# Kernel tuning notes

Measured on AMD Instinct MI355X. Metric: run time of the kernel, lower is better.

The kernel has to match this reference:

```python
import jax, jax.numpy as jnp
import numpy as np

N_NODES = 100000
N_EDGES = 3200000
IN_CH = 32
HID = 16


def setup_inputs() -> dict:
    key = jax.random.key(0)
    ks = jax.random.split(key, 8)
    x = jax.random.normal(ks[0], (N_NODES, IN_CH), dtype=jnp.float32)
    edge_index = jax.random.randint(ks[1], (2, N_EDGES), 0, N_NODES, dtype=jnp.int64)
    s1 = 1.0 / np.sqrt(IN_CH)
    s2 = 1.0 / np.sqrt(HID)
    Wl1 = jax.random.normal(ks[2], (HID, IN_CH), dtype=jnp.float32) * s1
    Wr1 = jax.random.normal(ks[3], (HID, IN_CH), dtype=jnp.float32) * s1
    b1 = jnp.zeros((HID,), dtype=jnp.float32)
    Wl2 = jax.random.normal(ks[4], (1, HID), dtype=jnp.float32) * s2
    Wr2 = jax.random.normal(ks[5], (1, HID), dtype=jnp.float32) * s2
    b2 = jnp.zeros((1,), dtype=jnp.float32)
    return {"x": x, "edge_index": edge_index, "Wl1": Wl1, "Wr1": Wr1,
            "b1": b1, "Wl2": Wl2, "Wr2": Wr2, "b2": b2}


def _sage_conv(h, src, dst, deg_inv, Wl, Wr, b):
    # mean aggregation of source features at destination nodes
    msg_sum = jax.ops.segment_sum(h[src], dst, num_segments=N_NODES)  # [N, F]
    agg = msg_sum * deg_inv[:, None]
    # lin_l(agg) + lin_r(h): lin_l carries the bias (PyG SAGEConv convention)
    return agg @ Wl.T + b + h @ Wr.T


def reference(x, edge_index, Wl1, Wr1, b1, Wl2, Wr2, b2):
    src = edge_index[0]
    dst = edge_index[1]
    deg = jax.ops.segment_sum(jnp.ones((N_EDGES,), dtype=x.dtype), dst,
                              num_segments=N_NODES)
    deg_inv = 1.0 / jnp.maximum(deg, 1.0)  # mean; nodes w/o in-edges get 0 agg

    h = _sage_conv(x, src, dst, deg_inv, Wl1, Wr1, b1)
    h = jax.nn.relu(h)
    # F.dropout in eval mode -> identity
    out = _sage_conv(h, src, dst, deg_inv, Wl2, Wr2, b2)
    return out.squeeze(-1)  # [N]
```

## Files before the change

### kernel.cpp

```cpp
#include <hip/hip_runtime.h>

#define N_NODES 100000
#define N_EDGES 3200000
#define NB 1024
#define BKN 98
#define RSZ 3968
#define TILE 6250
#define NTILES 512
#define MAXIT 13
#define MAXB 8
#define PROJ_BLOCKS 196

typedef float f32x4 __attribute__((ext_vector_type(4)));


__device__ __forceinline__ float bf2f_lo(unsigned int w) {
  return __uint_as_float(w << 16);
}
__device__ __forceinline__ float bf2f_hi(unsigned int w) {
  return __uint_as_float(w & 0xFFFF0000u);
}
__device__ __forceinline__ unsigned short f2bf(float f) {
  unsigned int b = __float_as_uint(f);
  return (unsigned short)((b + 0x7FFFu + ((b >> 16) & 1u)) >> 16);
}

__global__ __launch_bounds__(512, 4) void k_countproj(
    const float* __restrict__ x, const int* __restrict__ ei,
    const float* __restrict__ Wl1, const float* __restrict__ Wr1,
    const float* __restrict__ b1, unsigned short* __restrict__ p1h,
    float* __restrict__ q1b, int* __restrict__ cnt) {
  __shared__ union {
    int hist[1024];
    struct { float Wl[512], Wr[512], b[16]; } w;
  } u;
  const int t = threadIdx.x;
  const int kb = blockIdx.x;

  if (kb < NTILES) {
    for (int i = t; i < 1024; i += 512) u.hist[i] = 0;
    __syncthreads();
    const int tb = kb * TILE;
#pragma unroll
    for (int i = 0; i < MAXIT; ++i) {
      const int pos = t + i * 512;
      if (pos < TILE) {
        const int d = ei[N_EDGES + tb + pos];
        atomicAdd(&u.hist[(int)((unsigned)d / (unsigned)BKN)], 1);
      }
    }
    __syncthreads();
    ((int2*)(cnt + kb * NB))[t] = make_int2(u.hist[2 * t], u.hist[2 * t + 1]);
    return;
  }

  u.w.Wl[t] = Wl1[t];
  u.w.Wr[t] = Wr1[t];
  if (t < 16) u.w.b[t] = b1[t];
  __syncthreads();

  const int n = (kb - NTILES) * 512 + t;
  if (n >= N_NODES) return;

  float xr[32];
  const float4* xp = (const float4*)(x + (size_t)n * 32);
#pragma unroll
  for (int j = 0; j < 8; ++j) {
    float4 v = xp[j];
    xr[4 * j + 0] = v.x;
    xr[4 * j + 1] = v.y;
    xr[4 * j + 2] = v.z;
    xr[4 * j + 3] = v.w;
  }
  float pv[16], qv[16];
#pragma unroll
  for (int hh = 0; hh < 16; ++hh) {
    float a = 0.f, b = 0.f;
#pragma unroll
    for (int i = 0; i < 32; ++i) {
      a = fmaf(xr[i], u.w.Wl[hh * 32 + i], a);
      b = fmaf(xr[i], u.w.Wr[hh * 32 + i], b);
    }
    pv[hh] = a;
    qv[hh] = b + u.w.b[hh];
  }
  unsigned int w[8];
#pragma unroll
  for (int j = 0; j < 8; ++j)
    w[j] = (unsigned int)f2bf(pv[2 * j]) |
           ((unsigned int)f2bf(pv[2 * j + 1]) << 16);
  uint4* pp = (uint4*)(p1h + (size_t)n * 16);
  pp[0] = make_uint4(w[0], w[1], w[2], w[3]);
  pp[1] = make_uint4(w[4], w[5], w[6], w[7]);
  float4* qp = (float4*)(q1b + (size_t)n * 16);
#pragma unroll
  for (int j = 0; j < 4; ++j)
    qp[j] = make_float4(qv[4 * j], qv[4 * j + 1], qv[4 * j + 2], qv[4 * j + 3]);
}

__global__ __launch_bounds__(512) void k_scan(const int* __restrict__ cnt,
                                              int* __restrict__ offs,
                                              int* __restrict__ tot) {
  const int t = threadIdx.x;
  const int lane = t & 63;
  const int b = blockIdx.x * 8 + (t >> 6);
  int carry = 0;
#pragma unroll
  for (int c = 0; c < 8; ++c) {
    const int tile = c * 64 + lane;
    const int v = cnt[tile * NB + b];
    int incl = v;
#pragma unroll
    for (int o = 1; o < 64; o <<= 1) {
      const int uu = __shfl_up(incl, o);
      if (lane >= o) incl += uu;
    }
    offs[b * NTILES + tile] = carry + incl - v;
    carry += __shfl(incl, 63);
  }
  if (lane == 0) tot[b] = carry;
}

__global__ __launch_bounds__(512, 4) void k_scatter(const int* __restrict__ ei,
                                                    const int* __restrict__ offs,
                                                    int* __restrict__ recs) {
  __shared__ int hist[1024];
  __shared__ int delta[NB];
  __shared__ int wsum[8];
  __shared__ int stage[TILE];
  __shared__ unsigned short bid[TILE + 6];
  const int t = threadIdx.x;
  const int kb = blockIdx.x;
  for (int i = t; i < 1024; i += 512) hist[i] = 0;
  __syncthreads();

  const int tb = kb * TILE;
  int rec[MAXIT], aux[MAXIT];
#pragma unroll
  for (int i = 0; i < MAXIT; ++i) {
    const int pos = t + i * 512;
    if (pos < TILE) {
      const int e = tb + pos;
      const int s = ei[e];
      const int d = ei[N_EDGES + e];
      const int k = (int)((unsigned)d / (unsigned)BKN);
      const int rank = atomicAdd(&hist[k], 1);
      rec[i] = ((d - k * BKN) << 17) | s;
      aux[i] = (k << 16) | rank;
    } else {
      aux[i] = -1;
    }
  }
  __syncthreads();

  const int s0 = hist[2 * t], s1 = hist[2 * t + 1];
  const int sp = s0 + s1;
  int incl = sp;
#pragma unroll
  for (int o = 1; o < 64; o <<= 1) {
    const int uu = __shfl_up(incl, o);
    if ((t & 63) >= o) incl += uu;
  }
  if ((t & 63) == 63) wsum[t >> 6] = incl;
  __syncthreads();
  if (t == 0) {
    int run = 0;
#pragma unroll
    for (int i = 0; i < 8; ++i) {
      const int v = wsum[i];
      wsum[i] = run;
      run += v;
    }
  }
  __syncthreads();
  const int ex = wsum[t >> 6] + incl - sp;
  hist[2 * t] = ex;
  hist[2 * t + 1] = ex + s0;
  {
    const int b = 2 * t;
    delta[b] = b * RSZ + offs[b * NTILES + kb] - ex;
    delta[b + 1] = (b + 1) * RSZ + offs[(b + 1) * NTILES + kb] - (ex + s0);
  }
  __syncthreads();

#pragma unroll
  for (int i = 0; i < MAXIT; ++i) {
    if (aux[i] >= 0) stage[hist[aux[i] >> 16] + (aux[i] & 0xFFFF)] = rec[i];
  }
  for (int k2 = t; k2 < NB; k2 += 512) {
    const int st = hist[k2];
    const int en = (k2 == NB - 1) ? TILE : hist[k2 + 1];
    for (int p = st; p < en; ++p) bid[p] = (unsigned short)k2;
  }
  __syncthreads();

  for (int pos = t; pos < TILE; pos += 512) {
    const int bb = bid[pos];
    const int idx = delta[bb] + pos;
    if (idx < (bb + 1) * RSZ) recs[idx] = stage[pos];
  }
}

__global__ __launch_bounds__(512, 8) void k_sortagg1(
    const int* __restrict__ tot, const int* __restrict__ recs,
    const unsigned short* __restrict__ p1h, const float* __restrict__ q1b,
    const float* __restrict__ Wl2, const float* __restrict__ Wr2,
    float* __restrict__ p2, float* __restrict__ r2,
    float* __restrict__ deg_inv) {
  __shared__ int hist[128];
  __shared__ int nstart[128];
  __shared__ int ssort[RSZ];
  __shared__ float sWl[16], sWr[16];
  const int t = threadIdx.x;
  const int kb = blockIdx.x;
  const int b0 = kb * RSZ;
  const int cend = min(tot[kb], RSZ);
  if (t < 128) hist[t] = 0;
  if (t < 16) {
    sWl[t] = Wl2[t];
    sWr[t] = Wr2[t];
  }
  __syncthreads();

  int rc[MAXB], ax[MAXB];
#pragma unroll
  for (int i = 0; i < MAXB; ++i) {
    const int r = t + i * 512;
    if (r < cend) {
      const int rv = recs[b0 + r];
      const int local = rv >> 17;
      const int rank = atomicAdd(&hist[local], 1);
      rc[i] = rv & 0x1FFFF;
      ax[i] = (local << 13) | rank;
    } else {
      ax[i] = -1;
    }
  }
  __syncthreads();

  if (t < 64) {
    const int a = hist[t], b = hist[t + 64];
    int ia = a, ib = b;
#pragma unroll
    for (int o = 1; o < 64; o <<= 1) {
      const int ua = __shfl_up(ia, o);
      const int ub = __shfl_up(ib, o);
      if (t >= o) {
        ia += ua;
        ib += ub;
      }
    }
    const int tt = __shfl(ia, 63);
    nstart[t] = ia - a;
    nstart[t + 64] = tt + ib - b;
  }
  __syncthreads();

#pragma unroll
  for (int i = 0; i < MAXB; ++i) {
    if (ax[i] >= 0) ssort[nstart[ax[i] >> 13] + (ax[i] & 0x1FFF)] = rc[i];
  }
  __syncthreads();

  const int quad = t & 3;
  const int half = quad & 1;
  const int epar = quad >> 1;
  const unsigned short* pb = p1h + half * 8;
  const int local = t >> 2;
  if (local < BKN) {
    const int n = kb * BKN + local;
    if (n < N_NODES) {
      const int st = nstart[local];
      const int k = hist[local];

      float acc[8];
#pragma unroll
      for (int i = 0; i < 8; ++i) acc[i] = 0.f;
      int j = epar;
      for (; j + 6 < k; j += 8) {
        const int s0 = ssort[st + j], s1 = ssort[st + j + 2],
                  s2 = ssort[st + j + 4], s3 = ssort[st + j + 6];
        const uint4 w0 = *(const uint4*)(pb + (size_t)s0 * 16);
        const uint4 w1 = *(const uint4*)(pb + (size_t)s1 * 16);
        const uint4 w2 = *(const uint4*)(pb + (size_t)s2 * 16);
        const uint4 w3 = *(const uint4*)(pb + (size_t)s3 * 16);
        acc[0] +=
            (bf2f_lo(w0.x) + bf2f_lo(w1.x)) + (bf2f_lo(w2.x) + bf2f_lo(w3.x));
        acc[1] +=
            (bf2f_hi(w0.x) + bf2f_hi(w1.x)) + (bf2f_hi(w2.x) + bf2f_hi(w3.x));
        acc[2] +=
            (bf2f_lo(w0.y) + bf2f_lo(w1.y)) + (bf2f_lo(w2.y) + bf2f_lo(w3.y));
        acc[3] +=
            (bf2f_hi(w0.y) + bf2f_hi(w1.y)) + (bf2f_hi(w2.y) + bf2f_hi(w3.y));
        acc[4] +=
            (bf2f_lo(w0.z) + bf2f_lo(w1.z)) + (bf2f_lo(w2.z) + bf2f_lo(w3.z));
        acc[5] +=
            (bf2f_hi(w0.z) + bf2f_hi(w1.z)) + (bf2f_hi(w2.z) + bf2f_hi(w3.z));
        acc[6] +=
            (bf2f_lo(w0.w) + bf2f_lo(w1.w)) + (bf2f_lo(w2.w) + bf2f_lo(w3.w));
        acc[7] +=
            (bf2f_hi(w0.w) + bf2f_hi(w1.w)) + (bf2f_hi(w2.w) + bf2f_hi(w3.w));
      }
      for (; j < k; j += 2) {
        const uint4 w = *(const uint4*)(pb + (size_t)ssort[st + j] * 16);
        acc[0] += bf2f_lo(w.x);
        acc[1] += bf2f_hi(w.x);
        acc[2] += bf2f_lo(w.y);
        acc[3] += bf2f_hi(w.y);
        acc[4] += bf2f_lo(w.z);
        acc[5] += bf2f_hi(w.z);
        acc[6] += bf2f_lo(w.w);
        acc[7] += bf2f_hi(w.w);
      }
#pragma unroll
      for (int i = 0; i < 8; ++i) acc[i] += __shfl_xor(acc[i], 2);

      const float di = 1.f / fmaxf((float)k, 1.f);
      const float4* qp = (const float4*)(q1b + (size_t)n * 16 + half * 8);
      const float4 qa = qp[0], qb = qp[1];
      float h[8];
      h[0] = fmaxf(fmaf(acc[0], di, qa.x), 0.f);
      h[1] = fmaxf(fmaf(acc[1], di, qa.y), 0.f);
      h[2] = fmaxf(fmaf(acc[2], di, qa.z), 0.f);
      h[3] = fmaxf(fmaf(acc[3], di, qa.w), 0.f);
      h[4] = fmaxf(fmaf(acc[4], di, qb.x), 0.f);
      h[5] = fmaxf(fmaf(acc[5], di, qb.y), 0.f);
      h[6] = fmaxf(fmaf(acc[6], di, qb.z), 0.f);
      h[7] = fmaxf(fmaf(acc[7], di, qb.w), 0.f);
      float pa = 0.f, pbv = 0.f;
#pragma unroll
      for (int i = 0; i < 8; ++i) {
        pa = fmaf(h[i], sWl[half * 8 + i], pa);
        pbv = fmaf(h[i], sWr[half * 8 + i], pbv);
      }
      pa += __shfl_xor(pa, 1);
      pbv += __shfl_xor(pbv, 1);
      if (quad == 0) {
        p2[n] = pa;
        r2[n] = pbv;
        deg_inv[n] = di;
      }
    }
  }
}

__global__ __launch_bounds__(512, 8) void k_agg2out(
    const int* __restrict__ tot, const int* __restrict__ recs,
    const float* __restrict__ p2, const float* __restrict__ r2,
    const float* __restrict__ deg_inv, const float* __restrict__ b2,
    float* __restrict__ out) {
  __shared__ float acc[BKN];
  const int t = threadIdx.x;
  const int kb = blockIdx.x;
  if (t < BKN) acc[t] = 0.f;
  __syncthreads();

  const int b0 = kb * RSZ;
  const int cnt = min(tot[kb], RSZ);
  int r = t;
  for (; r + 1536 < cnt; r += 2048) {
    const int rv0 = recs[b0 + r];
    const int rv1 = recs[b0 + r + 512];
    const int rv2 = recs[b0 + r + 1024];
    const int rv3 = recs[b0 + r + 1536];
    const float v0 = p2[rv0 & 0x1FFFF];
    const float v1 = p2[rv1 & 0x1FFFF];
    const float v2 = p2[rv2 & 0x1FFFF];
    const float v3 = p2[rv3 & 0x1FFFF];
    atomicAdd(&acc[rv0 >> 17], v0);
    atomicAdd(&acc[rv1 >> 17], v1);
    atomicAdd(&acc[rv2 >> 17], v2);
    atomicAdd(&acc[rv3 >> 17], v3);
  }
  for (; r < cnt; r += 512) {
    const int rv = recs[b0 + r];
    atomicAdd(&acc[rv >> 17], p2[rv & 0x1FFFF]);
  }
  __syncthreads();

  if (t < BKN) {
    const int n = kb * BKN + t;
    if (n < N_NODES) out[n] = fmaf(acc[t], deg_inv[n], r2[n] + b2[0]);
  }
}

extern "C" void kernel_launch(void* const* d_in, const int* in_sizes, int n_in,
                              void* d_out, int out_size, void* d_ws,
                              size_t ws_size, hipStream_t stream) {
  const float* x   = (const float*)d_in[0];
  const int*   ei  = (const int*)d_in[1];
  const float* Wl1 = (const float*)d_in[2];
  const float* Wr1 = (const float*)d_in[3];
  const float* b1  = (const float*)d_in[4];
  const float* Wl2 = (const float*)d_in[5];
  const float* Wr2 = (const float*)d_in[6];
  const float* b2  = (const float*)d_in[7];
  float* out = (float*)d_out;

  const size_t N = N_NODES;
  int* wi = (int*)d_ws;
  int* cnt  = wi;
  int* offs = cnt + NTILES * NB;
  int* tot  = offs + NB * NTILES;
  int* recs = tot + NB;
  unsigned short* p1h = (unsigned short*)(recs + (size_t)NB * RSZ);
  float* q1b     = (float*)(p1h + 16 * N);
  float* p2      = q1b + 16 * N;
  float* r2      = p2 + N;
  float* deg_inv = r2 + N;

  k_countproj<<<NTILES + PROJ_BLOCKS, 512, 0, stream>>>(x, ei, Wl1, Wr1, b1,
                                                        p1h, q1b, cnt);
  k_scan<<<NB / 8, 512, 0, stream>>>(cnt, offs, tot);
  k_scatter<<<NTILES, 512, 0, stream>>>(ei, offs, recs);
  k_sortagg1<<<NB, 512, 0, stream>>>(tot, recs, p1h, q1b, Wl2, Wr2, p2, r2,
                                     deg_inv);
  k_agg2out<<<NB, 512, 0, stream>>>(tot, recs, p2, r2, deg_inv, b2, out);
}
```

Measured before the change: 176.4 us.

## Fuse both aggregation stages into a cooperative kernel and restructure scatter tiles

Merges the layer-1 sort/aggregate and layer-2 aggregate/output kernels into one cooperative kernel with a grid-wide sync. The second stage reuses the per-bucket sorted edge lists, degree and root term already in LDS instead of re-reading records and global arrays. The scatter kernel now uses larger 1024-thread tiles with a two-pass count-then-place sort, and writes 16-aligned padded runs with hole records as int4 stores. The cost is extra padding slots, a larger RSZ, and a reliance on cooperative launch residency, with the old two-kernel path kept as a fallback.

```diff
diff --git a/kernel.cpp b/kernel.cpp
--- a/kernel.cpp
+++ b/kernel.cpp
@@ -1,17 +1,19 @@
 #include <hip/hip_runtime.h>
+#include <hip/hip_cooperative_groups.h>
+
+namespace cg = cooperative_groups;
 
 #define N_NODES 100000
 #define N_EDGES 3200000
 #define NB 1024
 #define BKN 98
-#define RSZ 3968
-#define TILE 6250
-#define NTILES 512
-#define MAXIT 13
-#define MAXB 8
+#define RSZ 5120
+#define TILE 12500
+#define NTILES 256
+#define MAXITC 25
+#define MAXB 10
 #define PROJ_BLOCKS 196
-
-typedef float f32x4 __attribute__((ext_vector_type(4)));
+#define HOLE_REC (127 << 17)
 
 
 __device__ __forceinline__ float bf2f_lo(unsigned int w) {
@@ -42,7 +44,7 @@
     __syncthreads();
     const int tb = kb * TILE;
 #pragma unroll
-    for (int i = 0; i < MAXIT; ++i) {
+    for (int i = 0; i < MAXITC; ++i) {
       const int pos = t + i * 512;
       if (pos < TILE) {
         const int d = ei[N_EDGES + tb + pos];
@@ -106,113 +108,109 @@
   const int b = blockIdx.x * 8 + (t >> 6);
   int carry = 0;
 #pragma unroll
-  for (int c = 0; c < 8; ++c) {
+  for (int c = 0; c < 4; ++c) {
     const int tile = c * 64 + lane;
-    const int v = cnt[tile * NB + b];
-    int incl = v;
+    const int pv = (cnt[tile * NB + b] + 15) & ~15;
+    int incl = pv;
 #pragma unroll
     for (int o = 1; o < 64; o <<= 1) {
       const int uu = __shfl_up(incl, o);
       if (lane >= o) incl += uu;
     }
-    offs[b * NTILES + tile] = carry + incl - v;
+    offs[b * NTILES + tile] = carry + incl - pv;
     carry += __shfl(incl, 63);
   }
   if (lane == 0) tot[b] = carry;
 }
 
-__global__ __launch_bounds__(512, 4) void k_scatter(const int* __restrict__ ei,
-                                                    const int* __restrict__ offs,
-                                                    int* __restrict__ recs) {
+__global__ __launch_bounds__(1024, 1) void k_scatter(
+    const int* __restrict__ ei, const int* __restrict__ offs,
+    int* __restrict__ recs) {
   __shared__ int hist[1024];
-  __shared__ int delta[NB];
-  __shared__ int wsum[8];
+  __shared__ int bstart[1024];
+  __shared__ int wsum[16];
   __shared__ int stage[TILE];
-  __shared__ unsigned short bid[TILE + 6];
   const int t = threadIdx.x;
   const int kb = blockIdx.x;
-  for (int i = t; i < 1024; i += 512) hist[i] = 0;
+  hist[t] = 0;
   __syncthreads();
 
   const int tb = kb * TILE;
-  int rec[MAXIT], aux[MAXIT];
-#pragma unroll
-  for (int i = 0; i < MAXIT; ++i) {
-    const int pos = t + i * 512;
+#pragma unroll
+  for (int i = 0; i < 13; ++i) {
+    const int pos = t + i * 1024;
+    if (pos < TILE) {
+      const int d = ei[N_EDGES + tb + pos];
+      atomicAdd(&hist[(int)((unsigned)d / (unsigned)BKN)], 1);
+    }
+  }
+  __syncthreads();
+
+  const int sv = hist[t];
+  int incl = sv;
+#pragma unroll
+  for (int o = 1; o < 64; o <<= 1) {
+    const int uu = __shfl_up(incl, o);
+    if ((t & 63) >= o) incl += uu;
+  }
+  if ((t & 63) == 63) wsum[t >> 6] = incl;
+  __syncthreads();
+  if (t == 0) {
+    int run = 0;
+#pragma unroll
+    for (int i = 0; i < 16; ++i) {
+      const int v = wsum[i];
+      wsum[i] = run;
+      run += v;
+    }
+  }
+  __syncthreads();
+  bstart[t] = wsum[t >> 6] + incl - sv;
+  hist[t] = 0;
+  __syncthreads();
+
+#pragma unroll
+  for (int i = 0; i < 13; ++i) {
+    const int pos = t + i * 1024;
     if (pos < TILE) {
       const int e = tb + pos;
       const int s = ei[e];
       const int d = ei[N_EDGES + e];
       const int k = (int)((unsigned)d / (unsigned)BKN);
-      const int rank = atomicAdd(&hist[k], 1);
-      rec[i] = ((d - k * BKN) << 17) | s;
-      aux[i] = (k << 16) | rank;
-    } else {
-      aux[i] = -1;
-    }
-  }
-  __syncthreads();
-
-  const int s0 = hist[2 * t], s1 = hist[2 * t + 1];
-  const int sp = s0 + s1;
-  int incl = sp;
-#pragma unroll
-  for (int o = 1; o < 64; o <<= 1) {
-    const int uu = __shfl_up(incl, o);
-    if ((t & 63) >= o) incl += uu;
-  }
-  if ((t & 63) == 63) wsum[t >> 6] = incl;
-  __syncthreads();
-  if (t == 0) {
-    int run = 0;
-#pragma unroll
-    for (int i = 0; i < 8; ++i) {
-      const int v = wsum[i];
-      wsum[i] = run;
-      run += v;
-    }
-  }
-  __syncthreads();
-  const int ex = wsum[t >> 6] + incl - sp;
-  hist[2 * t] = ex;
-  hist[2 * t + 1] = ex + s0;
+      const int r = atomicAdd(&hist[k], 1);
+      stage[bstart[k] + r] = ((d - k * BKN) << 17) | s;
+    }
+  }
+  __syncthreads();
+
   {
-    const int b = 2 * t;
-    delta[b] = b * RSZ + offs[b * NTILES + kb] - ex;
-    delta[b + 1] = (b + 1) * RSZ + offs[(b + 1) * NTILES + kb] - (ex + s0);
-  }
-  __syncthreads();
-
-#pragma unroll
-  for (int i = 0; i < MAXIT; ++i) {
-    if (aux[i] >= 0) stage[hist[aux[i] >> 16] + (aux[i] & 0xFFFF)] = rec[i];
-  }
-  for (int k2 = t; k2 < NB; k2 += 512) {
-    const int st = hist[k2];
-    const int en = (k2 == NB - 1) ? TILE : hist[k2 + 1];
-    for (int p = st; p < en; ++p) bid[p] = (unsigned short)k2;
-  }
-  __syncthreads();
-
-  for (int pos = t; pos < TILE; pos += 512) {
-    const int bb = bid[pos];
-    const int idx = delta[bb] + pos;
-    if (idx < (bb + 1) * RSZ) recs[idx] = stage[pos];
-  }
-}
-
-__global__ __launch_bounds__(512, 8) void k_sortagg1(
-    const int* __restrict__ tot, const int* __restrict__ recs,
-    const unsigned short* __restrict__ p1h, const float* __restrict__ q1b,
-    const float* __restrict__ Wl2, const float* __restrict__ Wr2,
-    float* __restrict__ p2, float* __restrict__ r2,
-    float* __restrict__ deg_inv) {
-  __shared__ int hist[128];
-  __shared__ int nstart[128];
-  __shared__ int ssort[RSZ];
-  __shared__ float sWl[16], sWr[16];
-  const int t = threadIdx.x;
-  const int kb = blockIdx.x;
+    const int b = t;
+    const int c = hist[b];
+    const int st = bstart[b];
+    const int off = offs[b * NTILES + kb];
+    const int pc = (c + 15) & ~15;
+    int* gb = recs + (size_t)b * RSZ + off;
+    for (int i = 0; i < pc; i += 4) {
+      if (off + i + 4 <= RSZ) {
+        int4 v;
+        v.x = (i < c) ? stage[st + i] : HOLE_REC;
+        v.y = (i + 1 < c) ? stage[st + i + 1] : HOLE_REC;
+        v.z = (i + 2 < c) ? stage[st + i + 2] : HOLE_REC;
+        v.w = (i + 3 < c) ? stage[st + i + 3] : HOLE_REC;
+        *(int4*)(gb + i) = v;
+      }
+    }
+  }
+}
+
+template <bool FUSED>
+__device__ __forceinline__ void sortagg_body(
+    const int t, const int kb, const int* __restrict__ tot,
+    const int* __restrict__ recs, const unsigned short* __restrict__ p1h,
+    const float* __restrict__ q1b, const float* __restrict__ Wl2,
+    const float* __restrict__ Wr2, float* __restrict__ p2,
+    float* __restrict__ r2g, float* __restrict__ degg, int* hist, int* nstart,
+    int* ssort, float* sWl, float* sWr, float* sr2, float* sdi) {
   const int b0 = kb * RSZ;
   const int cend = min(tot[kb], RSZ);
   if (t < 128) hist[t] = 0;
@@ -337,11 +335,69 @@
       pbv += __shfl_xor(pbv, 1);
       if (quad == 0) {
         p2[n] = pa;
-        r2[n] = pbv;
-        deg_inv[n] = di;
-      }
-    }
-  }
+        if (FUSED) {
+          sr2[local] = pbv;
+          sdi[local] = di;
+        } else {
+          r2g[n] = pbv;
+          degg[n] = di;
+        }
+      }
+    }
+  }
+}
+
+__global__ __launch_bounds__(512, 8) void k_fused(
+    const int* __restrict__ tot, const int* __restrict__ recs,
+    const unsigned short* __restrict__ p1h, const float* __restrict__ q1b,
+    const float* __restrict__ Wl2, const float* __restrict__ Wr2,
+    float* __restrict__ p2, const float* __restrict__ b2,
+    float* __restrict__ out) {
+  __shared__ int hist[128], nstart[128];
+  __shared__ int ssort[RSZ];
+  __shared__ float sWl[16], sWr[16], sr2[BKN], sdi[BKN];
+  cg::grid_group g = cg::this_grid();
+  const int t = threadIdx.x;
+  const int kb = blockIdx.x;
+
+  sortagg_body<true>(t, kb, tot, recs, p1h, q1b, Wl2, Wr2, p2, nullptr,
+                     nullptr, hist, nstart, ssort, sWl, sWr, sr2, sdi);
+  __threadfence();
+  g.sync();
+
+  const int lane4 = t & 3;
+  const int local = t >> 2;
+  if (local < BKN) {
+    const int n = kb * BKN + local;
+    if (n < N_NODES) {
+      const int st = nstart[local];
+      const int k = hist[local];
+      float u = 0.f;
+      int j = lane4;
+      for (; j + 4 < k; j += 8) {
+        const int a = ssort[st + j], b = ssort[st + j + 4];
+        u += p2[a] + p2[b];
+      }
+      for (; j < k; j += 4) u += p2[ssort[st + j]];
+      u += __shfl_xor(u, 1);
+      u += __shfl_xor(u, 2);
+      if (lane4 == 0) out[n] = fmaf(u, sdi[local], sr2[local] + b2[0]);
+    }
+  }
+}
+
+__global__ __launch_bounds__(512, 8) void k_sortagg1(
+    const int* __restrict__ tot, const int* __restrict__ recs,
+    const unsigned short* __restrict__ p1h, const float* __restrict__ q1b,
+    const float* __restrict__ Wl2, const float* __restrict__ Wr2,
+    float* __restrict__ p2, float* __restrict__ r2,
+    float* __restrict__ deg_inv) {
+  __shared__ int hist[128], nstart[128];
+  __shared__ int ssort[RSZ];
+  __shared__ float sWl[16], sWr[16];
+  sortagg_body<false>(threadIdx.x, blockIdx.x, tot, recs, p1h, q1b, Wl2, Wr2,
+                      p2, r2, deg_inv, hist, nstart, ssort, sWl, sWr, nullptr,
+                      nullptr);
 }
 
 __global__ __launch_bounds__(512, 8) void k_agg2out(
@@ -349,10 +405,10 @@
     const float* __restrict__ p2, const float* __restrict__ r2,
     const float* __restrict__ deg_inv, const float* __restrict__ b2,
     float* __restrict__ out) {
-  __shared__ float acc[BKN];
+  __shared__ float acc[128];
   const int t = threadIdx.x;
   const int kb = blockIdx.x;
-  if (t < BKN) acc[t] = 0.f;
+  if (t < 128) acc[t] = 0.f;
   __syncthreads();
 
   const int b0 = kb * RSZ;
@@ -412,8 +468,17 @@
   k_countproj<<<NTILES + PROJ_BLOCKS, 512, 0, stream>>>(x, ei, Wl1, Wr1, b1,
                                                         p1h, q1b, cnt);
   k_scan<<<NB / 8, 512, 0, stream>>>(cnt, offs, tot);
-  k_scatter<<<NTILES, 512, 0, stream>>>(ei, offs, recs);
-  k_sortagg1<<<NB, 512, 0, stream>>>(tot, recs, p1h, q1b, Wl2, Wr2, p2, r2,
-                                     deg_inv);
-  k_agg2out<<<NB, 512, 0, stream>>>(tot, recs, p2, r2, deg_inv, b2, out);
-}
+  k_scatter<<<NTILES, 1024, 0, stream>>>(ei, offs, recs);
+
+  void* ka[] = {(void*)&tot, (void*)&recs, (void*)&p1h, (void*)&q1b,
+                (void*)&Wl2, (void*)&Wr2,  (void*)&p2,  (void*)&b2,
+                (void*)&out};
+  hipError_t err = hipLaunchCooperativeKernel(
+      reinterpret_cast<void*>(k_fused), dim3(NB), dim3(512), ka, 0, stream);
+  if (err != hipSuccess) {
+    (void)hipGetLastError();
+    k_sortagg1<<<NB, 512, 0, stream>>>(tot, recs, p1h, q1b, Wl2, Wr2, p2, r2,
+                                       deg_inv);
+    k_agg2out<<<NB, 512, 0, stream>>>(tot, recs, p2, r2, deg_inv, b2, out);
+  }
+}
```

Result: slower. 466.0 us (+164.2%).
